# Performance work log

Hardware: AMD Instinct MI355X
Metric: run time of the kernel (lower is better)

The kernel has to match this reference:

```python
import jax, jax.numpy as jnp
import numpy as np

N = 1048576
N_GRID = 256
DX = 1.0 / N_GRID
INV_DX = float(N_GRID)
DT = 2e-5
P_VOL = (DX * 0.5) ** 2
P_RHO = 1.0
P_MASS = P_VOL * P_RHO
E_MOD = 1000.0
NU = 0.2
MU_0 = E_MOD / (2.0 * (1.0 + NU))
LAM_0 = E_MOD * NU / ((1.0 + NU) * (1.0 - 2.0 * NU))
GRAVITY = 50.0


def setup_inputs() -> dict:
    key = jax.random.key(0)
    k = jax.random.split(key, 5)
    x = 0.1 + 0.8 * jax.random.uniform(k[0], (N, 2), dtype=jnp.float32)
    v = 0.1 * jax.random.normal(k[1], (N, 2), dtype=jnp.float32)
    C = 0.5 * jax.random.normal(k[2], (N, 2, 2), dtype=jnp.float32)
    F = jnp.eye(2, dtype=jnp.float32)[None] + 0.1 * jax.random.normal(k[3], (N, 2, 2), dtype=jnp.float32)
    material = jax.random.randint(k[4], (N,), 0, 3, dtype=jnp.int32)
    Jp = jnp.ones((N,), dtype=jnp.float32)
    return {"x": x, "v": v, "C": C, "F": F, "material": material, "Jp": Jp}


def reference(x, v, C, F, material, Jp):
    dt, inv_dx, dx = DT, INV_DX, DX
    base = jnp.floor(x * inv_dx - 0.5).astype(jnp.int32)          # [N,2]
    fx = x * inv_dx - base.astype(x.dtype)                        # [N,2]
    # quadratic B-spline weights, stacked over the 3 taps -> [3,N,2]
    w = jnp.stack([0.5 * (1.5 - fx) ** 2,
                   0.75 - (fx - 1.0) ** 2,
                   0.5 * (fx - 0.5) ** 2], axis=0)

    # deformation gradient update
    F = F + dt * jnp.einsum('nij,njk->nik', C, F)

    h = jnp.exp(10.0 * (1.0 - Jp))
    h = jnp.where(material == 1, 0.3, h)
    mu = jnp.where(material == 0, 0.0, MU_0 * h)
    lam = LAM_0 * h

    # per-particle 2x2 SVD (original pads to 3x3 and slices back)
    U, sig, Vh = jnp.linalg.svd(F)

    # snow plasticity: clamp singular values, track Jp
    clamped = jnp.clip(sig, 1.0 - 2.5e-2, 1.0 + 4.5e-3)
    is_snow = material == 2
    Jp = jnp.where(is_snow, Jp * jnp.prod(sig / clamped, axis=-1), Jp)
    sig = jnp.where(is_snow[:, None], clamped, sig)

    J = jnp.prod(sig, axis=-1)
    eye2 = jnp.eye(2, dtype=x.dtype)
    F_fluid = eye2[None] * jnp.sqrt(J)[:, None, None]             # J^(1/n_dim), n_dim=2
    F_snow = jnp.einsum('nij,nj,njk->nik', U, sig, Vh)
    F = jnp.where((material == 0)[:, None, None], F_fluid,
                  jnp.where(is_snow[:, None, None], F_snow, F))

    R = jnp.einsum('nij,njk->nik', U, Vh)
    stress = (2.0 * mu[:, None, None] * jnp.einsum('nij,nkj->nik', F - R, F)
              + eye2[None] * (lam * J * (J - 1.0))[:, None, None])
    stress = (-dt * P_VOL * 4.0 * inv_dx ** 2) * stress
    affine = stress + P_MASS * C                                   # [N,2,2]

    # ---- P2G scatter over the 3x3 stencil (vectorized over 9 taps) ----
    offs = jnp.array([[i, j] for i in range(3) for j in range(3)], dtype=jnp.int32)  # [9,2]
    weight = w[offs[:, 0], :, 0] * w[offs[:, 1], :, 1]             # [9,N]
    target = base[None, :, :] + offs[:, None, :]                   # [9,N,2]
    idx = target[..., 0] * N_GRID + target[..., 1]                 # [9,N]
    flat_idx = idx.reshape(-1)
    NG2 = N_GRID * N_GRID

    v_add = P_MASS * v - jnp.einsum('nij,nj->ni', affine, x)       # [N,2]
    grid_v = jax.ops.segment_sum((weight[..., None] * v_add[None]).reshape(-1, 2),
                                 flat_idx, num_segments=NG2).reshape(N_GRID, N_GRID, 2)
    grid_affine = jax.ops.segment_sum((weight[..., None, None] * affine[None]).reshape(-1, 4),
                                      flat_idx, num_segments=NG2).reshape(N_GRID, N_GRID, 2, 2)
    grid_m = jax.ops.segment_sum((weight * P_MASS).reshape(-1),
                                 flat_idx, num_segments=NG2).reshape(N_GRID, N_GRID)

    grid_x = jnp.stack(jnp.meshgrid(jnp.arange(N_GRID), jnp.arange(N_GRID), indexing='ij'),
                       axis=-1).astype(x.dtype) * dx               # [G,G,2]
    grid_v = grid_v + jnp.einsum('abij,abj->abi', grid_affine, grid_x)

    # grid ops: momentum -> velocity, gravity, boundary clamps
    m = grid_m[..., None]
    grid_v = jnp.where(m > 0, grid_v / jnp.maximum(m, 1e-12), grid_v)
    grid_v = grid_v.at[:, :, 1].add(-dt * GRAVITY)
    grid_v = grid_v.at[:3, :, 0].max(0.0)
    grid_v = grid_v.at[-2:, :, 0].min(0.0)
    grid_v = grid_v.at[:, :3, 1].max(0.0)
    grid_v = grid_v.at[:, -2:, 1].min(0.0)

    # ---- G2P gather ----
    gvf = grid_v.reshape(NG2, 2)
    g_v = gvf[idx]                                                 # [9,N,2]
    new_v = jnp.sum(weight[..., None] * g_v, axis=0)               # [N,2]
    pos = target.astype(x.dtype) * dx                              # [9,N,2]
    new_C = jnp.sum(weight[..., None, None] * g_v[..., :, None] * pos[..., None, :], axis=0)
    new_C = (new_C - new_v[..., None] * x[:, None, :]) * (4.0 * inv_dx ** 2)

    x = x + dt * new_v
    return (x, new_v, new_C, F, material, Jp)
```

## Files before the change

### kernel.cpp

```cpp
#include <hip/hip_runtime.h>

#define NG 256
#define NG2 (NG*NG)

constexpr float DX      = 1.0f / 256.0f;
constexpr float INV_DX  = 256.0f;
constexpr float DT      = 2e-5f;
constexpr float P_VOL   = (1.0f/512.0f) * (1.0f/512.0f);
constexpr float P_MASS  = P_VOL;
constexpr float MU_0    = 1000.0f / (2.0f * 1.2f);
constexpr float LAM_0   = 1000.0f * 0.2f / (1.2f * 0.6f);
constexpr float GRAV    = 50.0f;

__device__ __forceinline__ int bin_of(float px, float py) {
    int bx = (int)floorf(px * INV_DX - 0.5f);
    int by = (int)floorf(py * INV_DX - 0.5f);
    bx = min(max(bx, 0), NG - 1);
    by = min(max(by, 0), NG - 1);
    return (bx << 8) | by;
}

__device__ __forceinline__ float bw(float t) {
    float at = fabsf(t);
    float a  = fmaxf(1.5f - at, 0.0f);
    float w1 = 0.75f - t * t;
    float w2 = 0.5f * a * a;
    return (at < 0.5f) ? w1 : w2;
}


__global__ __launch_bounds__(256) void binrank_kernel(
    const float* __restrict__ x, int* __restrict__ counts, int* __restrict__ rank, int n)
{
    int i = blockIdx.x * blockDim.x + threadIdx.x;
    if (i >= n) return;
    float2 p = ((const float2*)x)[i];
    int b = bin_of(p.x, p.y);
    rank[i] = atomicAdd(&counts[b], 1);
}

__global__ __launch_bounds__(256) void scan1_kernel(
    const int* __restrict__ counts, int* __restrict__ starts, int* __restrict__ bsum)
{
    __shared__ int tmp[256];
    int t = threadIdx.x, b = blockIdx.x;
    int v = counts[b * 256 + t];
    tmp[t] = v;
    __syncthreads();
    #pragma unroll
    for (int off = 1; off < 256; off <<= 1) {
        int add = (t >= off) ? tmp[t - off] : 0;
        __syncthreads();
        tmp[t] += add;
        __syncthreads();
    }
    starts[b * 256 + t] = tmp[t] - v;
    if (t == 255) bsum[b] = tmp[255];
}

__global__ __launch_bounds__(256) void scan2_kernel(int* __restrict__ bsum)
{
    __shared__ int tmp[256];
    int t = threadIdx.x;
    int v = bsum[t];
    tmp[t] = v;
    __syncthreads();
    #pragma unroll
    for (int off = 1; off < 256; off <<= 1) {
        int add = (t >= off) ? tmp[t - off] : 0;
        __syncthreads();
        tmp[t] += add;
        __syncthreads();
    }
    bsum[t] = tmp[t] - v;
}

__global__ __launch_bounds__(256) void scan3_kernel(
    int* __restrict__ starts, const int* __restrict__ bsum, int n)
{
    int i = blockIdx.x * blockDim.x + threadIdx.x;
    if (i < NG2) starts[i] += bsum[i >> 8];
    if (i == 0) starts[NG2] = n;
}


__device__ __forceinline__ void particle_update(
    int i,
    const float2* __restrict__ x2, const float2* __restrict__ v2,
    const float4* __restrict__ C4, const float4* __restrict__ F4,
    const int* __restrict__ mat, const float* __restrict__ Jp,
    const int* __restrict__ starts, const int* __restrict__ rank,
    float4* __restrict__ srec0, float4* __restrict__ srec1,
    float4* __restrict__ F_out4, float* __restrict__ mat_out, float* __restrict__ Jp_out)
{
    float2 xp = x2[i];
    float2 vp = v2[i];
    float4 Cp = C4[i];
    float4 Fp = F4[i];
    int    m  = mat[i];
    float  jp = Jp[i];

    float px = xp.x, py = xp.y;
    float C00 = Cp.x, C01 = Cp.y, C10 = Cp.z, C11 = Cp.w;
    float a = Fp.x, b = Fp.y, c = Fp.z, d = Fp.w;

    float na = a + DT*(C00*a + C01*c);
    float nb = b + DT*(C00*b + C01*d);
    float nc = c + DT*(C10*a + C11*c);
    float nd = d + DT*(C10*b + C11*d);
    a = na; b = nb; c = nc; d = nd;

    float h = expf(10.0f * (1.0f - jp));
    if (m == 1) h = 0.3f;
    float mu  = (m == 0) ? 0.0f : MU_0 * h;
    float lam = LAM_0 * h;

    float S00 = a*a + c*c, S01 = a*b + c*d, S11 = b*b + d*d;
    float mh = 0.5f*(S00 + S11), dh = 0.5f*(S00 - S11);
    float delta = sqrtf(dh*dh + S01*S01);
    float sig1 = sqrtf(fmaxf(mh + delta, 0.0f));
    float sig2 = sqrtf(fmaxf(mh - delta, 0.0f));
    float e0, e1;
    if (dh >= 0.0f) { e0 = delta + dh; e1 = S01; }
    else            { e0 = S01;        e1 = delta - dh; }
    float elen = sqrtf(e0*e0 + e1*e1);
    float vc, vs;
    if (elen > 1e-30f) { float il = 1.0f/elen; vc = e0*il; vs = e1*il; }
    else               { vc = 1.0f; vs = 0.0f; }
    float inv1 = 1.0f / fmaxf(sig1, 1e-30f);
    float inv2 = 1.0f / fmaxf(sig2, 1e-30f);
    float u1x = ( a*vc + b*vs) * inv1, u1y = ( c*vc + d*vs) * inv1;
    float u2x = (-a*vs + b*vc) * inv2, u2y = (-c*vs + d*vc) * inv2;

    if (m == 2) {
        float c1 = fminf(fmaxf(sig1, 1.0f - 2.5e-2f), 1.0f + 4.5e-3f);
        float c2 = fminf(fmaxf(sig2, 1.0f - 2.5e-2f), 1.0f + 4.5e-3f);
        jp = jp * (sig1 / c1) * (sig2 / c2);
        sig1 = c1; sig2 = c2;
    }
    float J = sig1 * sig2;

    if (m == 0) {
        float s = sqrtf(J);
        a = s; b = 0.0f; c = 0.0f; d = s;
    } else if (m == 2) {
        a = sig1*u1x*vc - sig2*u2x*vs;
        b = sig1*u1x*vs + sig2*u2x*vc;
        c = sig1*u1y*vc - sig2*u2y*vs;
        d = sig1*u1y*vs + sig2*u2y*vc;
    }
    float R00 = u1x*vc - u2x*vs, R01 = u1x*vs + u2x*vc;
    float R10 = u1y*vc - u2y*vs, R11 = u1y*vs + u2y*vc;

    float k2mu = 2.0f * mu;
    float fr00 = a - R00, fr01 = b - R01, fr10 = c - R10, fr11 = d - R11;
    float ljj  = lam * J * (J - 1.0f);
    float st00 = k2mu*(fr00*a + fr01*b) + ljj;
    float st01 = k2mu*(fr00*c + fr01*d);
    float st10 = k2mu*(fr10*a + fr11*b);
    float st11 = k2mu*(fr10*c + fr11*d) + ljj;
    const float coef = -DT * P_VOL * 4.0f * INV_DX * INV_DX;
    float A00 = coef*st00 + P_MASS*C00;
    float A01 = coef*st01 + P_MASS*C01;
    float A10 = coef*st10 + P_MASS*C10;
    float A11 = coef*st11 + P_MASS*C11;

    float bx_ = P_MASS*vp.x - (A00*px + A01*py);
    float by_ = P_MASS*vp.y - (A10*px + A11*py);

    int bidx = bin_of(px, py);
    int sidx = starts[bidx] + rank[i];
    srec0[sidx] = make_float4(px * INV_DX, py * INV_DX, bx_, by_);
    srec1[sidx] = make_float4(A00, A01, A10, A11);

    F_out4[i]  = make_float4(a, b, c, d);
    mat_out[i] = (float)m;
    Jp_out[i]  = jp;
}

__global__ __launch_bounds__(256) void compute_scatter_kernel(
    const float* __restrict__ x, const float* __restrict__ v,
    const float* __restrict__ C, const float* __restrict__ F,
    const int* __restrict__ mat, const float* __restrict__ Jp,
    const int* __restrict__ starts, const int* __restrict__ rank,
    float4* __restrict__ srec0, float4* __restrict__ srec1,
    float* __restrict__ F_out, float* __restrict__ mat_out, float* __restrict__ Jp_out,
    int n)
{
    int t = blockIdx.x * blockDim.x + threadIdx.x;
    int half = n >> 1;
    const float2* x2 = (const float2*)x;
    const float2* v2 = (const float2*)v;
    const float4* C4 = (const float4*)C;
    const float4* F4 = (const float4*)F;
    float4* F_out4 = (float4*)F_out;

    if (t < half) {
        particle_update(t,        x2, v2, C4, F4, mat, Jp, starts, rank,
                        srec0, srec1, F_out4, mat_out, Jp_out);
        particle_update(t + half, x2, v2, C4, F4, mat, Jp, starts, rank,
                        srec0, srec1, F_out4, mat_out, Jp_out);
    } else if ((n & 1) && t == half) {
        particle_update(n - 1, x2, v2, C4, F4, mat, Jp, starts, rank,
                        srec0, srec1, F_out4, mat_out, Jp_out);
    }
}

__global__ __launch_bounds__(256) void gather_grid_kernel(
    const float4* __restrict__ srec0, const float4* __restrict__ srec1,
    const int* __restrict__ starts, float2* __restrict__ gv)
{
    int gtid  = blockIdx.x * blockDim.x + threadIdx.x;
    int cell  = gtid >> 3;
    int slice = gtid & 7;
    int gi = cell >> 8, gj = cell & (NG - 1);

    float fgi = (float)gi, fgj = (float)gj;
    float posx = fgi * DX, posy = fgj * DX;
    float msum = 0.0f, mvx = 0.0f, mvy = 0.0f;

    int i0 = max(gi - 2, 0);
    int j0 = max(gj - 2, 0);

    for (int bi = i0; bi <= gi; ++bi) {
        int row = bi << 8;
        int s = starts[row + j0];
        int e = starts[row + gj + 1];
        for (int k = s + slice; k < e; k += 16) {
            float4 r0 = srec0[k];
            float4 r1 = srec1[k];
            int k2 = k + 8;
            bool sec = (k2 < e);
            float4 q0, q1;
            if (sec) { q0 = srec0[k2]; q1 = srec1[k2]; }
            float w = bw(r0.x - fgi) * bw(r0.y - fgj);
            msum += w;
            mvx  += w * (r0.z + r1.x * posx + r1.y * posy);
            mvy  += w * (r0.w + r1.z * posx + r1.w * posy);
            if (sec) {
                float w2 = bw(q0.x - fgi) * bw(q0.y - fgj);
                msum += w2;
                mvx  += w2 * (q0.z + q1.x * posx + q1.y * posy);
                mvy  += w2 * (q0.w + q1.z * posx + q1.w * posy);
            }
        }
    }

    #pragma unroll
    for (int off = 1; off < 8; off <<= 1) {
        msum += __shfl_xor(msum, off);
        mvx  += __shfl_xor(mvx,  off);
        mvy  += __shfl_xor(mvy,  off);
    }

    if (slice == 0) {
        float mass = msum * P_MASS;
        float vx = mvx, vy = mvy;
        if (mass > 0.0f) {
            float im = 1.0f / fmaxf(mass, 1e-12f);
            vx *= im; vy *= im;
        }
        vy -= DT * GRAV;
        if (gi < 3)      vx = fmaxf(vx, 0.0f);
        if (gi >= NG-2)  vx = fminf(vx, 0.0f);
        if (gj < 3)      vy = fmaxf(vy, 0.0f);
        if (gj >= NG-2)  vy = fminf(vy, 0.0f);
        gv[cell] = make_float2(vx, vy);
    }
}

__global__ __launch_bounds__(256) void g2p_kernel(
    const float* __restrict__ x, const float2* __restrict__ gv,
    float* __restrict__ x_out, float* __restrict__ v_out, float* __restrict__ C_out,
    int n)
{
    int i = blockIdx.x * blockDim.x + threadIdx.x;
    if (i >= n) return;

    float2 xp = ((const float2*)x)[i];
    float px = xp.x, py = xp.y;
    float bxf = floorf(px * INV_DX - 0.5f), byf = floorf(py * INV_DX - 0.5f);
    float fx = px * INV_DX - bxf, fy = py * INV_DX - byf;
    float wxs[3] = { 0.5f*(1.5f-fx)*(1.5f-fx), 0.75f-(fx-1.0f)*(fx-1.0f), 0.5f*(fx-0.5f)*(fx-0.5f) };
    float wys[3] = { 0.5f*(1.5f-fy)*(1.5f-fy), 0.75f-(fy-1.0f)*(fy-1.0f), 0.5f*(fy-0.5f)*(fy-0.5f) };
    int bix = (int)bxf, biy = (int)byf;

    float nvx = 0.0f, nvy = 0.0f;
    float c00 = 0.0f, c01 = 0.0f, c10 = 0.0f, c11 = 0.0f;
    #pragma unroll
    for (int ii = 0; ii < 3; ++ii) {
        float posx = (bxf + (float)ii) * DX;
        int rowbase = (bix + ii) * NG + biy;
        #pragma unroll
        for (int jj = 0; jj < 3; ++jj) {
            float w = wxs[ii] * wys[jj];
            float posy = (byf + (float)jj) * DX;
            float2 g = gv[rowbase + jj];
            nvx += w * g.x; nvy += w * g.y;
            c00 += w * g.x * posx; c01 += w * g.x * posy;
            c10 += w * g.y * posx; c11 += w * g.y * posy;
        }
    }
    const float K = 4.0f * INV_DX * INV_DX;
    c00 = (c00 - nvx * px) * K; c01 = (c01 - nvx * py) * K;
    c10 = (c10 - nvy * px) * K; c11 = (c11 - nvy * py) * K;

    ((float2*)x_out)[i] = make_float2(px + DT * nvx, py + DT * nvy);
    ((float2*)v_out)[i] = make_float2(nvx, nvy);
    ((float4*)C_out)[i] = make_float4(c00, c01, c10, c11);
}

extern "C" void kernel_launch(void* const* d_in, const int* in_sizes, int n_in,
                              void* d_out, int out_size, void* d_ws, size_t ws_size,
                              hipStream_t stream) {
    const float* x   = (const float*)d_in[0];
    const float* v   = (const float*)d_in[1];
    const float* C   = (const float*)d_in[2];
    const float* F   = (const float*)d_in[3];
    const int*   mat = (const int*)d_in[4];
    const float* Jp  = (const float*)d_in[5];

    int n = in_sizes[0] / 2;

    float* out     = (float*)d_out;
    float* x_out   = out;
    float* v_out   = out + (size_t)2*n;
    float* C_out   = out + (size_t)4*n;
    float* F_out   = out + (size_t)8*n;
    float* mat_out = out + (size_t)12*n;
    float* Jp_out  = out + (size_t)13*n;

    int blocks = (n + 255) / 256;

    char* ws = (char*)d_ws;
    size_t off = 0;
    int* counts = (int*)(ws + off); off += (size_t)NG2 * 4;
    int* starts = (int*)(ws + off); off += (size_t)(NG2 + 1) * 4;
    int* bsum   = (int*)(ws + off); off += 256 * 4;
    int* rank   = (int*)(ws + off); off += (size_t)n * 4;
    off = (off + 15) & ~(size_t)15;
    float4* srec0 = (float4*)(ws + off); off += (size_t)n * 16;
    float4* srec1 = (float4*)(ws + off); off += (size_t)n * 16;
    float2* gv    = (float2*)(ws + off); off += (size_t)NG2 * 8;

    hipMemsetAsync(counts, 0, (size_t)NG2 * 4, stream);
    binrank_kernel<<<blocks, 256, 0, stream>>>(x, counts, rank, n);
    scan1_kernel<<<NG2/256, 256, 0, stream>>>(counts, starts, bsum);
    scan2_kernel<<<1, 256, 0, stream>>>(bsum);
    scan3_kernel<<<NG2/256, 256, 0, stream>>>(starts, bsum, n);
    int half_blocks = ((n + 1) / 2 + 255) / 256;
    compute_scatter_kernel<<<half_blocks, 256, 0, stream>>>(x, v, C, F, mat, Jp,
                                                            starts, rank, srec0, srec1,
                                                            F_out, mat_out, Jp_out, n);
    gather_grid_kernel<<<(NG2*8)/256, 256, 0, stream>>>(srec0, srec1, starts, gv);
    g2p_kernel<<<blocks, 256, 0, stream>>>(x, gv, x_out, v_out, C_out, n);
}
```

Before: 147.7 us.

## Interleave sorted particle records, use nontemporal stores, widen grid gather to 16 lanes

The two separate sorted-record arrays are merged into one interleaved 32-byte-per-particle array, so a gather reads adjacent float4 pairs. Record and per-particle output writes use nontemporal stores to reduce cache pollution. The compute kernel goes back to one particle per thread. The grid gather now uses 16 lanes per cell with a swizzled block order and loads all three bin-row ranges up front. The extra lanes and swizzle aim for more parallelism and better locality, at the cost of more shuffle reductions and idle lanes in sparse cells.

```diff
diff --git a/kernel.cpp b/kernel.cpp
--- a/kernel.cpp
+++ b/kernel.cpp
@@ -2,6 +2,8 @@
 
 #define NG 256
 #define NG2 (NG*NG)
+
+typedef float vfloat4 __attribute__((ext_vector_type(4)));
 
 constexpr float DX      = 1.0f / 256.0f;
 constexpr float INV_DX  = 256.0f;
@@ -28,6 +30,11 @@
     return (at < 0.5f) ? w1 : w2;
 }
 
+__device__ __forceinline__ void nt_store4(float4* dst, float a, float b, float c, float d) {
+    vfloat4 val = { a, b, c, d };
+    __builtin_nontemporal_store(val, reinterpret_cast<vfloat4*>(dst));
+}
+
 
 __global__ __launch_bounds__(256) void binrank_kernel(
     const float* __restrict__ x, int* __restrict__ counts, int* __restrict__ rank, int n)
@@ -84,19 +91,22 @@
 }
 
 
-__device__ __forceinline__ void particle_update(
-    int i,
-    const float2* __restrict__ x2, const float2* __restrict__ v2,
-    const float4* __restrict__ C4, const float4* __restrict__ F4,
+__global__ __launch_bounds__(256) void compute_scatter_kernel(
+    const float* __restrict__ x, const float* __restrict__ v,
+    const float* __restrict__ C, const float* __restrict__ F,
     const int* __restrict__ mat, const float* __restrict__ Jp,
     const int* __restrict__ starts, const int* __restrict__ rank,
-    float4* __restrict__ srec0, float4* __restrict__ srec1,
-    float4* __restrict__ F_out4, float* __restrict__ mat_out, float* __restrict__ Jp_out)
-{
-    float2 xp = x2[i];
-    float2 vp = v2[i];
-    float4 Cp = C4[i];
-    float4 Fp = F4[i];
+    float4* __restrict__ srec,
+    float4* __restrict__ F_out4, float* __restrict__ mat_out, float* __restrict__ Jp_out,
+    int n)
+{
+    int i = blockIdx.x * blockDim.x + threadIdx.x;
+    if (i >= n) return;
+
+    float2 xp = ((const float2*)x)[i];
+    float2 vp = ((const float2*)v)[i];
+    float4 Cp = ((const float4*)C)[i];
+    float4 Fp = ((const float4*)F)[i];
     int    m  = mat[i];
     float  jp = Jp[i];
 
@@ -168,86 +178,57 @@
     float bx_ = P_MASS*vp.x - (A00*px + A01*py);
     float by_ = P_MASS*vp.y - (A10*px + A11*py);
 
-    int bidx = bin_of(px, py);
-    int sidx = starts[bidx] + rank[i];
-    srec0[sidx] = make_float4(px * INV_DX, py * INV_DX, bx_, by_);
-    srec1[sidx] = make_float4(A00, A01, A10, A11);
-
-    F_out4[i]  = make_float4(a, b, c, d);
-    mat_out[i] = (float)m;
-    Jp_out[i]  = jp;
-}
-
-__global__ __launch_bounds__(256) void compute_scatter_kernel(
-    const float* __restrict__ x, const float* __restrict__ v,
-    const float* __restrict__ C, const float* __restrict__ F,
-    const int* __restrict__ mat, const float* __restrict__ Jp,
-    const int* __restrict__ starts, const int* __restrict__ rank,
-    float4* __restrict__ srec0, float4* __restrict__ srec1,
-    float* __restrict__ F_out, float* __restrict__ mat_out, float* __restrict__ Jp_out,
-    int n)
-{
-    int t = blockIdx.x * blockDim.x + threadIdx.x;
-    int half = n >> 1;
-    const float2* x2 = (const float2*)x;
-    const float2* v2 = (const float2*)v;
-    const float4* C4 = (const float4*)C;
-    const float4* F4 = (const float4*)F;
-    float4* F_out4 = (float4*)F_out;
-
-    if (t < half) {
-        particle_update(t,        x2, v2, C4, F4, mat, Jp, starts, rank,
-                        srec0, srec1, F_out4, mat_out, Jp_out);
-        particle_update(t + half, x2, v2, C4, F4, mat, Jp, starts, rank,
-                        srec0, srec1, F_out4, mat_out, Jp_out);
-    } else if ((n & 1) && t == half) {
-        particle_update(n - 1, x2, v2, C4, F4, mat, Jp, starts, rank,
-                        srec0, srec1, F_out4, mat_out, Jp_out);
-    }
+    int sidx = starts[bin_of(px, py)] + rank[i];
+    nt_store4(&srec[2*sidx],     px * INV_DX, py * INV_DX, bx_, by_);
+    nt_store4(&srec[2*sidx + 1], A00, A01, A10, A11);
+
+    nt_store4(&F_out4[i], a, b, c, d);
+    __builtin_nontemporal_store((float)m, &mat_out[i]);
+    __builtin_nontemporal_store(jp, &Jp_out[i]);
 }
 
 __global__ __launch_bounds__(256) void gather_grid_kernel(
-    const float4* __restrict__ srec0, const float4* __restrict__ srec1,
-    const int* __restrict__ starts, float2* __restrict__ gv)
-{
-    int gtid  = blockIdx.x * blockDim.x + threadIdx.x;
-    int cell  = gtid >> 3;
-    int slice = gtid & 7;
+    const float4* __restrict__ srec, const int* __restrict__ starts,
+    float2* __restrict__ gv)
+{
+    int bid  = blockIdx.x;
+    int swz  = (bid & 7) * (4096 / 8) + (bid >> 3);
+    int gtid  = swz * 256 + threadIdx.x;
+    int cell  = gtid >> 4;
+    int slice = gtid & 15;
     int gi = cell >> 8, gj = cell & (NG - 1);
 
     float fgi = (float)gi, fgj = (float)gj;
     float posx = fgi * DX, posy = fgj * DX;
     float msum = 0.0f, mvx = 0.0f, mvy = 0.0f;
 
-    int i0 = max(gi - 2, 0);
     int j0 = max(gj - 2, 0);
 
-    for (int bi = i0; bi <= gi; ++bi) {
-        int row = bi << 8;
-        int s = starts[row + j0];
-        int e = starts[row + gj + 1];
+    int sArr[3], eArr[3];
+    #pragma unroll
+    for (int t3 = 0; t3 < 3; ++t3) {
+        int bi = gi - 2 + t3;
+        bool valid = (bi >= 0);
+        int row = (valid ? bi : 0) << 8;
+        sArr[t3] = valid ? starts[row + j0] : 0;
+        eArr[t3] = valid ? starts[row + gj + 1] : 0;
+    }
+
+    #pragma unroll
+    for (int t3 = 0; t3 < 3; ++t3) {
+        int s = sArr[t3], e = eArr[t3];
         for (int k = s + slice; k < e; k += 16) {
-            float4 r0 = srec0[k];
-            float4 r1 = srec1[k];
-            int k2 = k + 8;
-            bool sec = (k2 < e);
-            float4 q0, q1;
-            if (sec) { q0 = srec0[k2]; q1 = srec1[k2]; }
+            float4 r0 = srec[2*k];
+            float4 r1 = srec[2*k + 1];
             float w = bw(r0.x - fgi) * bw(r0.y - fgj);
             msum += w;
             mvx  += w * (r0.z + r1.x * posx + r1.y * posy);
             mvy  += w * (r0.w + r1.z * posx + r1.w * posy);
-            if (sec) {
-                float w2 = bw(q0.x - fgi) * bw(q0.y - fgj);
-                msum += w2;
-                mvx  += w2 * (q0.z + q1.x * posx + q1.y * posy);
-                mvy  += w2 * (q0.w + q1.z * posx + q1.w * posy);
-            }
         }
     }
 
     #pragma unroll
-    for (int off = 1; off < 8; off <<= 1) {
+    for (int off = 1; off < 16; off <<= 1) {
         msum += __shfl_xor(msum, off);
         mvx  += __shfl_xor(mvx,  off);
         mvy  += __shfl_xor(mvy,  off);
@@ -338,20 +319,18 @@
     int* starts = (int*)(ws + off); off += (size_t)(NG2 + 1) * 4;
     int* bsum   = (int*)(ws + off); off += 256 * 4;
     int* rank   = (int*)(ws + off); off += (size_t)n * 4;
-    off = (off + 15) & ~(size_t)15;
-    float4* srec0 = (float4*)(ws + off); off += (size_t)n * 16;
-    float4* srec1 = (float4*)(ws + off); off += (size_t)n * 16;
-    float2* gv    = (float2*)(ws + off); off += (size_t)NG2 * 8;
+    off = (off + 63) & ~(size_t)63;
+    float4* srec = (float4*)(ws + off); off += (size_t)n * 32;
+    float2* gv   = (float2*)(ws + off); off += (size_t)NG2 * 8;
 
     hipMemsetAsync(counts, 0, (size_t)NG2 * 4, stream);
     binrank_kernel<<<blocks, 256, 0, stream>>>(x, counts, rank, n);
     scan1_kernel<<<NG2/256, 256, 0, stream>>>(counts, starts, bsum);
     scan2_kernel<<<1, 256, 0, stream>>>(bsum);
     scan3_kernel<<<NG2/256, 256, 0, stream>>>(starts, bsum, n);
-    int half_blocks = ((n + 1) / 2 + 255) / 256;
-    compute_scatter_kernel<<<half_blocks, 256, 0, stream>>>(x, v, C, F, mat, Jp,
-                                                            starts, rank, srec0, srec1,
-                                                            F_out, mat_out, Jp_out, n);
-    gather_grid_kernel<<<(NG2*8)/256, 256, 0, stream>>>(srec0, srec1, starts, gv);
+    compute_scatter_kernel<<<blocks, 256, 0, stream>>>(x, v, C, F, mat, Jp,
+                                                       starts, rank, srec,
+                                                       (float4*)F_out, mat_out, Jp_out, n);
+    gather_grid_kernel<<<(NG2*16)/256, 256, 0, stream>>>(srec, starts, gv);
     g2p_kernel<<<blocks, 256, 0, stream>>>(x, gv, x_out, v_out, C_out, n);
 }
```

Measured after the change: 179.7 us. 21.7% more time.
